# Optimization experiments

Measured on AMD Instinct MI355X. Metric: run time of the kernel, lower is better.

The kernel has to match this reference:

```python
import jax, jax.numpy as jnp
import numpy as np

N = 100_000      # nodes
E = 1_600_000    # directed edges (before self-loops)
F_IN = 128       # input node features
H = 4            # attention heads
C = 64           # hidden channels (concat=False -> heads averaged)
NEG_SLOPE = 0.2
BN_EPS = 1e-5


def setup_inputs() -> dict:
    key = jax.random.key(0)
    ks = jax.random.split(key, 16)
    s = 0.05
    return {
        "x": jax.random.normal(ks[0], (N, F_IN), dtype=jnp.float32),
        "edge_index": jax.random.randint(ks[1], (2, E), 0, N, dtype=jnp.int64),
        # GAT layer params: layer 0 has F_IN inputs, layers 1..2 have C inputs
        "W0": jax.random.normal(ks[2], (F_IN, H * C), dtype=jnp.float32) * s,
        "Wl": jax.random.normal(ks[3], (2, C, H * C), dtype=jnp.float32) * s,
        "att_src": jax.random.normal(ks[4], (3, H, C), dtype=jnp.float32) * s,
        "att_dst": jax.random.normal(ks[5], (3, H, C), dtype=jnp.float32) * s,
        "conv_bias": jnp.zeros((3, C), dtype=jnp.float32),
        # BatchNorm1d (inference: running stats)
        "bn_gamma": jnp.ones((3, C), dtype=jnp.float32),
        "bn_beta": jnp.zeros((3, C), dtype=jnp.float32),
        "bn_mean": jax.random.normal(ks[6], (3, C), dtype=jnp.float32) * 0.1,
        "bn_var": jax.random.uniform(ks[7], (3, C), dtype=jnp.float32, minval=0.5, maxval=1.5),
        # MLP head
        "lin1_w": jax.random.normal(ks[8], (C, C // 2), dtype=jnp.float32) * s,
        "lin1_b": jnp.zeros((C // 2,), dtype=jnp.float32),
        "lin2_w": jax.random.normal(ks[9], (C // 2, 1), dtype=jnp.float32) * s,
        "lin2_b": jnp.zeros((1,), dtype=jnp.float32),
    }


def _gat_layer(x, src, dst, W, a_src, a_dst, bias):
    # x: [N, Fin] -> h: [N, H, C]
    h = (x @ W).reshape(-1, H, C)
    # per-node attention logits, gathered per edge: [Etot, H]
    e_src = jnp.einsum("nhc,hc->nh", h, a_src)
    e_dst = jnp.einsum("nhc,hc->nh", h, a_dst)
    e = jax.nn.leaky_relu(e_src[src] + e_dst[dst], NEG_SLOPE)
    # softmax over incoming edges of each target node (self-loops guarantee non-empty)
    e_max = jax.ops.segment_max(e, dst, num_segments=N)
    w = jnp.exp(e - e_max[dst])                              # [Etot, H]
    denom = jax.ops.segment_sum(w, dst, num_segments=N)      # [N, H]
    # weighted scatter-add of gathered source features
    msg = h[src] * w[:, :, None]                             # [Etot, H, C]
    out = jax.ops.segment_sum(msg, dst, num_segments=N)      # [N, H, C]
    out = out / denom[:, :, None]
    return out.mean(axis=1) + bias                           # concat=False -> head mean


def reference(x, edge_index, W0, Wl, att_src, att_dst, conv_bias,
              bn_gamma, bn_beta, bn_mean, bn_var,
              lin1_w, lin1_b, lin2_w, lin2_b):
    # add self-loops (PyG GATConv default)
    loop = jnp.arange(N, dtype=edge_index.dtype)
    src = jnp.concatenate([edge_index[0], loop])
    dst = jnp.concatenate([edge_index[1], loop])

    Ws = [W0, Wl[0], Wl[1]]
    for l in range(3):
        x = _gat_layer(x, src, dst, Ws[l], att_src[l], att_dst[l], conv_bias[l])
        x = (x - bn_mean[l]) * (bn_gamma[l] / jnp.sqrt(bn_var[l] + BN_EPS)) + bn_beta[l]
        x = jax.nn.relu(x)  # dropout is identity in inference

    x = jax.nn.relu(x @ lin1_w + lin1_b)
    x = x @ lin2_w + lin2_b
    return x.squeeze(-1)
```

## Files before the change

### kernel.cpp

```cpp
#include <hip/hip_runtime.h>
#include <hip/hip_bf16.h>
#include <cstdint>

#define N_NODES 100000
#define N_EDGES 1600000
#define N_TOT   1700000
#define HEADS   4
#define CH      64
#define HC      256
#define NEG     0.2f
#define BNEPS   1e-5f

static __device__ __forceinline__ float lrelu(float x) {
    return x > 0.f ? x : NEG * x;
}
static __device__ __forceinline__ unsigned short f2bf(float f) {
    unsigned int u = __float_as_uint(f);
    unsigned int r = (u + 0x7fffu + ((u >> 16) & 1u)) >> 16;
    return (unsigned short)r;
}
static __device__ __forceinline__ float bflo(unsigned int v) { return __uint_as_float(v << 16); }
static __device__ __forceinline__ float bfhi(unsigned int v) { return __uint_as_float(v & 0xffff0000u); }

__global__ void detect_dtype(const int* ei32, int* flag) {
    int l = threadIdx.x;
    int v = ei32[2 * l + 1];
    unsigned long long b = __ballot(v == 0);
    if (l == 0) *flag = (__popcll(b) >= 48) ? 1 : 0;
}

static __device__ __forceinline__ int edge_at(const void* ei, int is64, long long pos) {
    if (is64) return (int)((const long long*)ei)[pos];
    return ((const int*)ei)[pos];
}

__global__ void hist_k(const void* ei, const int* flag, int* counts) {
    int e = blockIdx.x * blockDim.x + threadIdx.x;
    if (e >= N_TOT) return;
    int is64 = *flag;
    int d = (e < N_EDGES) ? edge_at(ei, is64, (long long)N_EDGES + e) : (e - N_EDGES);
    atomicAdd(&counts[d], 1);
}

__global__ void scan_block(const int* in, int* out, int* bsum) {
    __shared__ int sm[256];
    int t = threadIdx.x;
    int i = blockIdx.x * 256 + t;
    int v = (i < N_NODES) ? in[i] : 0;
    int acc = v;
    sm[t] = v; __syncthreads();
    for (int d = 1; d < 256; d <<= 1) {
        int add = (t >= d) ? sm[t - d] : 0;
        __syncthreads();
        acc += add; sm[t] = acc;
        __syncthreads();
    }
    if (i < N_NODES) out[i] = acc - v;
    if (t == 255) bsum[blockIdx.x] = acc;
}

__global__ void scan_bsum(int* bsum, int nb) {
    __shared__ int sm[512];
    int t = threadIdx.x;
    int v = (t < nb) ? bsum[t] : 0;
    int acc = v;
    sm[t] = v; __syncthreads();
    for (int d = 1; d < 512; d <<= 1) {
        int add = (t >= d) ? sm[t - d] : 0;
        __syncthreads();
        acc += add; sm[t] = acc;
        __syncthreads();
    }
    if (t < nb) bsum[t] = acc - v;
}

__global__ void scan_add(int* off, const int* bsum, int* fill) {
    int i = blockIdx.x * 256 + threadIdx.x;
    if (i < N_NODES) {
        int v = off[i] + bsum[blockIdx.x];
        off[i] = v; fill[i] = v;
    }
    if (i == 0) off[N_NODES] = N_TOT;
}

__global__ void scatter_k(const void* ei, const int* flag, int* fill, int* csr_src) {
    int e = blockIdx.x * blockDim.x + threadIdx.x;
    if (e >= N_TOT) return;
    int is64 = *flag;
    int s, d;
    if (e < N_EDGES) { s = edge_at(ei, is64, e); d = edge_at(ei, is64, (long long)N_EDGES + e); }
    else { s = e - N_EDGES; d = s; }
    int pos = atomicAdd(&fill[d], 1);
    csr_src[pos] = s;
}

__global__ __launch_bounds__(256) void gemm_fused_k(const float* __restrict__ A,
                                                    const float* __restrict__ W,
                                                    const float* __restrict__ as,
                                                    const float* __restrict__ ad,
                                                    unsigned short* __restrict__ hb,
                                                    float* __restrict__ es,
                                                    float* __restrict__ ed, int K) {
    __shared__ float As[16][68];
    __shared__ float Ws[16][64];
    int t = threadIdx.x;
    int bm = blockIdx.x * 64, bn = blockIdx.y * 64, head = blockIdx.y;
    int ty = t >> 4, tx = t & 15;
    float acc[4][4] = {{0.f}};
    int ar = t >> 2, ak = (t & 3) * 4;
    int wr = t >> 4, wc = (t & 15) * 4;

    for (int k0 = 0; k0 < K; k0 += 16) {
        float4 av = make_float4(0.f, 0.f, 0.f, 0.f);
        int grow = bm + ar;
        if (grow < N_NODES) av = *(const float4*)(A + (size_t)grow * K + k0 + ak);
        As[ak][ar] = av.x; As[ak + 1][ar] = av.y; As[ak + 2][ar] = av.z; As[ak + 3][ar] = av.w;
        *(float4*)(&Ws[wr][wc]) = *(const float4*)(W + (size_t)(k0 + wr) * HC + bn + wc);
        __syncthreads();
        #pragma unroll
        for (int kk = 0; kk < 16; ++kk) {
            float4 a  = *(const float4*)(&As[kk][ty * 4]);
            float4 bq = *(const float4*)(&Ws[kk][tx * 4]);
            acc[0][0] += a.x * bq.x; acc[0][1] += a.x * bq.y; acc[0][2] += a.x * bq.z; acc[0][3] += a.x * bq.w;
            acc[1][0] += a.y * bq.x; acc[1][1] += a.y * bq.y; acc[1][2] += a.y * bq.z; acc[1][3] += a.y * bq.w;
            acc[2][0] += a.z * bq.x; acc[2][1] += a.z * bq.y; acc[2][2] += a.z * bq.z; acc[2][3] += a.z * bq.w;
            acc[3][0] += a.w * bq.x; acc[3][1] += a.w * bq.y; acc[3][2] += a.w * bq.z; acc[3][3] += a.w * bq.w;
        }
        __syncthreads();
    }

    float4 asv = *(const float4*)(as + head * CH + tx * 4);
    float4 adv = *(const float4*)(ad + head * CH + tx * 4);

    #pragma unroll
    for (int r = 0; r < 4; ++r) {
        int grow = bm + ty * 4 + r;
        if (grow < N_NODES) {
            ushort4 hv;
            hv.x = f2bf(acc[r][0]); hv.y = f2bf(acc[r][1]);
            hv.z = f2bf(acc[r][2]); hv.w = f2bf(acc[r][3]);
            *(ushort4*)(hb + (size_t)grow * HC + bn + tx * 4) = hv;
        }
        float ps = acc[r][0] * asv.x + acc[r][1] * asv.y + acc[r][2] * asv.z + acc[r][3] * asv.w;
        float pd = acc[r][0] * adv.x + acc[r][1] * adv.y + acc[r][2] * adv.z + acc[r][3] * adv.w;
        #pragma unroll
        for (int d = 1; d < 16; d <<= 1) {
            ps += __shfl_xor(ps, d);
            pd += __shfl_xor(pd, d);
        }
        if (tx == 0 && grow < N_NODES) {
            es[(size_t)grow * 4 + head] = ps;
            ed[(size_t)grow * 4 + head] = pd;
        }
    }
}

__global__ __launch_bounds__(256) void aggregate_k(const unsigned short* __restrict__ h,
                                                   const float* __restrict__ es,
                                                   const float* __restrict__ ed,
                                                   const int* __restrict__ off,
                                                   const int* __restrict__ csr,
                                                   const float* __restrict__ bias,
                                                   const float* __restrict__ g,
                                                   const float* __restrict__ bb,
                                                   const float* __restrict__ mu,
                                                   const float* __restrict__ var,
                                                   float* __restrict__ xout) {
    __shared__ float wbuf[4][64][4];
    __shared__ int   sbuf[4][64];
    int wv = threadIdx.x >> 6;
    int lane = threadIdx.x & 63;
    int wid = blockIdx.x * 4 + wv;
    if (wid >= N_NODES) return;

    int s0 = off[wid], s1 = off[wid + 1];
    float4 edv = *(const float4*)(ed + (size_t)wid * 4);

    int half = lane >> 5;
    int sub  = lane & 31;
    int head = sub >> 3;
    float ds0 = 0.f, ds1 = 0.f, ds2 = 0.f, ds3 = 0.f;
    float a0 = 0.f, a1 = 0.f, a2 = 0.f, a3 = 0.f, a4 = 0.f, a5 = 0.f, a6 = 0.f, a7 = 0.f;

    for (int base = s0; base < s1; base += 64) {
        int e = base + lane;
        float w0 = 0.f, w1 = 0.f, w2 = 0.f, w3 = 0.f;
        int s = 0;
        if (e < s1) {
            s = csr[e];
            float4 ev = *(const float4*)(es + (size_t)s * 4);
            w0 = __expf(fminf(lrelu(ev.x + edv.x), 80.f));
            w1 = __expf(fminf(lrelu(ev.y + edv.y), 80.f));
            w2 = __expf(fminf(lrelu(ev.z + edv.z), 80.f));
            w3 = __expf(fminf(lrelu(ev.w + edv.w), 80.f));
        }
        ds0 += w0; ds1 += w1; ds2 += w2; ds3 += w3;
        *(float4*)(&wbuf[wv][lane][0]) = make_float4(w0, w1, w2, w3);
        sbuf[wv][lane] = s;
        asm volatile("" ::: "memory");

        int cnt = min(64, s1 - base);
        for (int j = 0; j < cnt; j += 2) {
            int jj = j + half;
            if (jj < cnt) {
                int   ss = sbuf[wv][jj];
                float wm = wbuf[wv][jj][head];
                uint4 hv = *(const uint4*)(h + (size_t)ss * HC + sub * 8);
                a0 = fmaf(wm, bflo(hv.x), a0); a1 = fmaf(wm, bfhi(hv.x), a1);
                a2 = fmaf(wm, bflo(hv.y), a2); a3 = fmaf(wm, bfhi(hv.y), a3);
                a4 = fmaf(wm, bflo(hv.z), a4); a5 = fmaf(wm, bfhi(hv.z), a5);
                a6 = fmaf(wm, bflo(hv.w), a6); a7 = fmaf(wm, bfhi(hv.w), a7);
            }
        }
        asm volatile("" ::: "memory");
    }

    a0 += __shfl_xor(a0, 32); a1 += __shfl_xor(a1, 32);
    a2 += __shfl_xor(a2, 32); a3 += __shfl_xor(a3, 32);
    a4 += __shfl_xor(a4, 32); a5 += __shfl_xor(a5, 32);
    a6 += __shfl_xor(a6, 32); a7 += __shfl_xor(a7, 32);

    #pragma unroll
    for (int d = 1; d < 64; d <<= 1) {
        ds0 += __shfl_xor(ds0, d); ds1 += __shfl_xor(ds1, d);
        ds2 += __shfl_xor(ds2, d); ds3 += __shfl_xor(ds3, d);
    }
    float den = head == 0 ? ds0 : head == 1 ? ds1 : head == 2 ? ds2 : ds3;
    float inv = 1.f / den;
    a0 *= inv; a1 *= inv; a2 *= inv; a3 *= inv;
    a4 *= inv; a5 *= inv; a6 *= inv; a7 *= inv;

    a0 += __shfl_xor(a0, 8);  a1 += __shfl_xor(a1, 8);
    a2 += __shfl_xor(a2, 8);  a3 += __shfl_xor(a3, 8);
    a4 += __shfl_xor(a4, 8);  a5 += __shfl_xor(a5, 8);
    a6 += __shfl_xor(a6, 8);  a7 += __shfl_xor(a7, 8);
    a0 += __shfl_xor(a0, 16); a1 += __shfl_xor(a1, 16);
    a2 += __shfl_xor(a2, 16); a3 += __shfl_xor(a3, 16);
    a4 += __shfl_xor(a4, 16); a5 += __shfl_xor(a5, 16);
    a6 += __shfl_xor(a6, 16); a7 += __shfl_xor(a7, 16);

    if (lane < 8) {
        int c = lane * 8;
        float av[8] = {a0, a1, a2, a3, a4, a5, a6, a7};
        float4 bi0 = *(const float4*)(bias + c), bi1 = *(const float4*)(bias + c + 4);
        float4 gv0 = *(const float4*)(g + c),    gv1 = *(const float4*)(g + c + 4);
        float4 bv0 = *(const float4*)(bb + c),   bv1 = *(const float4*)(bb + c + 4);
        float4 mv0 = *(const float4*)(mu + c),   mv1 = *(const float4*)(mu + c + 4);
        float4 vv0 = *(const float4*)(var + c),  vv1 = *(const float4*)(var + c + 4);
        float bia[8] = {bi0.x, bi0.y, bi0.z, bi0.w, bi1.x, bi1.y, bi1.z, bi1.w};
        float gg[8]  = {gv0.x, gv0.y, gv0.z, gv0.w, gv1.x, gv1.y, gv1.z, gv1.w};
        float be[8]  = {bv0.x, bv0.y, bv0.z, bv0.w, bv1.x, bv1.y, bv1.z, bv1.w};
        float mm[8]  = {mv0.x, mv0.y, mv0.z, mv0.w, mv1.x, mv1.y, mv1.z, mv1.w};
        float vv[8]  = {vv0.x, vv0.y, vv0.z, vv0.w, vv1.x, vv1.y, vv1.z, vv1.w};
        float o[8];
        #pragma unroll
        for (int k = 0; k < 8; ++k) {
            float t0 = (av[k] * 0.25f + bia[k] - mm[k]) * (gg[k] * rsqrtf(vv[k] + BNEPS)) + be[k];
            o[k] = fmaxf(t0, 0.f);
        }
        *(float4*)(xout + (size_t)wid * CH + c)     = make_float4(o[0], o[1], o[2], o[3]);
        *(float4*)(xout + (size_t)wid * CH + c + 4) = make_float4(o[4], o[5], o[6], o[7]);
    }
}

__global__ __launch_bounds__(256) void mlp_k(const float* __restrict__ x,
                                             const float* __restrict__ w1,
                                             const float* __restrict__ b1,
                                             const float* __restrict__ w2,
                                             const float* __restrict__ b2,
                                             float* __restrict__ out) {
    __shared__ float w1s[CH * 32];
    __shared__ float w2s[32];
    __shared__ float b1s[32];
    int t = threadIdx.x;
    for (int i = t; i < CH * 32; i += 256) w1s[i] = w1[i];
    if (t < 32) { w2s[t] = w2[t]; b1s[t] = b1[t]; }
    __syncthreads();
    int n = blockIdx.x * 256 + t;
    if (n >= N_NODES) return;
    float y[32];
    #pragma unroll
    for (int j = 0; j < 32; ++j) y[j] = b1s[j];
    const float* xr = x + (size_t)n * CH;
    for (int c4 = 0; c4 < 16; ++c4) {
        float4 xv = *(const float4*)(xr + c4 * 4);
        const float* wr = &w1s[c4 * 4 * 32];
        #pragma unroll
        for (int j = 0; j < 32; ++j)
            y[j] += xv.x * wr[j] + xv.y * wr[32 + j] + xv.z * wr[64 + j] + xv.w * wr[96 + j];
    }
    float o = b2[0];
    #pragma unroll
    for (int j = 0; j < 32; ++j) o += fmaxf(y[j], 0.f) * w2s[j];
    out[n] = o;
}

extern "C" void kernel_launch(void* const* d_in, const int* in_sizes, int n_in,
                              void* d_out, int out_size, void* d_ws, size_t ws_size,
                              hipStream_t stream) {
    const float* x0    = (const float*)d_in[0];
    const void*  ei    = d_in[1];
    const float* W0    = (const float*)d_in[2];
    const float* Wl    = (const float*)d_in[3];
    const float* asrc  = (const float*)d_in[4];
    const float* adst  = (const float*)d_in[5];
    const float* cbias = (const float*)d_in[6];
    const float* bng   = (const float*)d_in[7];
    const float* bnb   = (const float*)d_in[8];
    const float* bnm   = (const float*)d_in[9];
    const float* bnv   = (const float*)d_in[10];
    const float* l1w   = (const float*)d_in[11];
    const float* l1b   = (const float*)d_in[12];
    const float* l2w   = (const float*)d_in[13];
    const float* l2b   = (const float*)d_in[14];
    float* out = (float*)d_out;

    char* p = (char*)d_ws;
    auto alloc = [&](size_t bytes) { char* r = p; p += (bytes + 255) & ~(size_t)255; return r; };
    unsigned short* hb = (unsigned short*)alloc((size_t)N_NODES * HC * 2);
    float* xA   = (float*)alloc((size_t)N_NODES * CH * 4);
    float* xB   = (float*)alloc((size_t)N_NODES * CH * 4);
    float* es   = (float*)alloc((size_t)N_NODES * 4 * 4);
    float* ed   = (float*)alloc((size_t)N_NODES * 4 * 4);
    int* counts = (int*)alloc((size_t)N_NODES * 4);
    int* off    = (int*)alloc((size_t)(N_NODES + 1) * 4);
    int* fill   = (int*)alloc((size_t)N_NODES * 4);
    int* bsum   = (int*)alloc(512 * 4);
    int* flag   = (int*)alloc(256);
    int* csr    = (int*)alloc((size_t)N_TOT * 4);

    int nbScan = (N_NODES + 255) / 256;
    hipMemsetAsync(counts, 0, (size_t)N_NODES * 4, stream);
    detect_dtype<<<1, 64, 0, stream>>>((const int*)ei, flag);
    hist_k<<<(N_TOT + 255) / 256, 256, 0, stream>>>(ei, flag, counts);
    scan_block<<<nbScan, 256, 0, stream>>>(counts, off, bsum);
    scan_bsum<<<1, 512, 0, stream>>>(bsum, nbScan);
    scan_add<<<nbScan, 256, 0, stream>>>(off, bsum, fill);
    scatter_k<<<(N_TOT + 255) / 256, 256, 0, stream>>>(ei, flag, fill, csr);

    const float* xin = x0;
    int K = 128;
    const float* W = W0;
    float* xbufs[2] = {xA, xB};
    for (int l = 0; l < 3; ++l) {
        dim3 gg((N_NODES + 63) / 64, HC / 64);
        gemm_fused_k<<<gg, 256, 0, stream>>>(xin, W, asrc + l * HC, adst + l * HC,
                                             hb, es, ed, K);
        float* xo = xbufs[l & 1];
        aggregate_k<<<(N_NODES + 3) / 4, 256, 0, stream>>>(hb, es, ed, off, csr,
            cbias + l * CH, bng + l * CH, bnb + l * CH, bnm + l * CH, bnv + l * CH, xo);
        xin = xo;
        K = CH;
        W = Wl + (size_t)l * CH * HC;
    }
    mlp_k<<<(N_NODES + 255) / 256, 256, 0, stream>>>(xin, l1w, l1b, l2w, l2b, out);
}
```

Before: 848.9 us.

## Use bf16 MFMA GEMM, partitioned CSR build, and wider per-lane aggregation

The FP32 SIMT GEMM is replaced by a bf16 MFMA 16x16x32 kernel with swizzled LDS tiles. Each block now covers all four heads, and the weights are converted to bf16 per layer. The CSR build first converts edges to int32, then runs the histogram and scatter in destination-range partitions so atomics stay local in cache. Aggregation now has each lane load 16 bf16 channels per edge and process four edges at a time. Rounding the inputs and weights to bf16 adds precision loss, and the partitioned passes read the edge list eight times.

```diff
diff --git a/kernel.cpp b/kernel.cpp
--- a/kernel.cpp
+++ b/kernel.cpp
@@ -10,6 +10,12 @@
 #define HC      256
 #define NEG     0.2f
 #define BNEPS   1e-5f
+#define NPART   8
+#define PART_N  12500
+#define CHUNK_E 16384
+
+typedef __attribute__((ext_vector_type(8))) short short8;
+typedef __attribute__((ext_vector_type(4))) float f32x4;
 
 static __device__ __forceinline__ float lrelu(float x) {
     return x > 0.f ? x : NEG * x;
@@ -34,12 +40,28 @@
     return ((const int*)ei)[pos];
 }
 
-__global__ void hist_k(const void* ei, const int* flag, int* counts) {
-    int e = blockIdx.x * blockDim.x + threadIdx.x;
+__global__ void convert_k(const void* ei, const int* flag, int* src32, int* dst32) {
+    int e = blockIdx.x * 256 + threadIdx.x;
     if (e >= N_TOT) return;
     int is64 = *flag;
-    int d = (e < N_EDGES) ? edge_at(ei, is64, (long long)N_EDGES + e) : (e - N_EDGES);
-    atomicAdd(&counts[d], 1);
+    if (e < N_EDGES) {
+        src32[e] = edge_at(ei, is64, e);
+        dst32[e] = edge_at(ei, is64, (long long)N_EDGES + e);
+    } else {
+        int v = e - N_EDGES;
+        src32[e] = v; dst32[e] = v;
+    }
+}
+
+__global__ void hist_part_k(const int* __restrict__ dst32, int* __restrict__ counts) {
+    int part = blockIdx.x & (NPART - 1), chunk = blockIdx.x / NPART;
+    int lo = part * PART_N, hi = lo + PART_N;
+    int base = chunk * CHUNK_E;
+    int end = min(base + CHUNK_E, N_TOT);
+    for (int i = base + threadIdx.x; i < end; i += 256) {
+        int d = dst32[i];
+        if (d >= lo && d < hi) atomicAdd(&counts[d], 1);
+    }
 }
 
 __global__ void scan_block(const int* in, int* out, int* bsum) {
@@ -83,75 +105,135 @@
     if (i == 0) off[N_NODES] = N_TOT;
 }
 
-__global__ void scatter_k(const void* ei, const int* flag, int* fill, int* csr_src) {
-    int e = blockIdx.x * blockDim.x + threadIdx.x;
-    if (e >= N_TOT) return;
-    int is64 = *flag;
-    int s, d;
-    if (e < N_EDGES) { s = edge_at(ei, is64, e); d = edge_at(ei, is64, (long long)N_EDGES + e); }
-    else { s = e - N_EDGES; d = s; }
-    int pos = atomicAdd(&fill[d], 1);
-    csr_src[pos] = s;
-}
-
-__global__ __launch_bounds__(256) void gemm_fused_k(const float* __restrict__ A,
-                                                    const float* __restrict__ W,
-                                                    const float* __restrict__ as,
-                                                    const float* __restrict__ ad,
-                                                    unsigned short* __restrict__ hb,
-                                                    float* __restrict__ es,
-                                                    float* __restrict__ ed, int K) {
-    __shared__ float As[16][68];
-    __shared__ float Ws[16][64];
+__global__ void scatter_part_k(const int* __restrict__ src32, const int* __restrict__ dst32,
+                               int* __restrict__ fill, int* __restrict__ csr) {
+    int part = blockIdx.x & (NPART - 1), chunk = blockIdx.x / NPART;
+    int lo = part * PART_N, hi = lo + PART_N;
+    int base = chunk * CHUNK_E;
+    int end = min(base + CHUNK_E, N_TOT);
+    for (int i = base + threadIdx.x; i < end; i += 256) {
+        int d = dst32[i];
+        if (d >= lo && d < hi) {
+            int s = src32[i];
+            int pos = atomicAdd(&fill[d], 1);
+            csr[pos] = s;
+        }
+    }
+}
+
+__global__ void wconv_k(const float* __restrict__ w, unsigned short* __restrict__ wb, int n) {
+    int i = blockIdx.x * 256 + threadIdx.x;
+    if (i < n) wb[i] = f2bf(w[i]);
+}
+
+template<int K>
+__global__ __launch_bounds__(256) void gemm_mfma_k(const float* __restrict__ A,
+                                                   const unsigned short* __restrict__ Wb,
+                                                   const float* __restrict__ as,
+                                                   const float* __restrict__ ad,
+                                                   unsigned short* __restrict__ hb,
+                                                   float* __restrict__ es,
+                                                   float* __restrict__ ed) {
+    __shared__ unsigned short Bs[256 * K];
+    __shared__ unsigned short As[64 * K];
     int t = threadIdx.x;
-    int bm = blockIdx.x * 64, bn = blockIdx.y * 64, head = blockIdx.y;
-    int ty = t >> 4, tx = t & 15;
-    float acc[4][4] = {{0.f}};
-    int ar = t >> 2, ak = (t & 3) * 4;
-    int wr = t >> 4, wc = (t & 15) * 4;
-
-    for (int k0 = 0; k0 < K; k0 += 16) {
-        float4 av = make_float4(0.f, 0.f, 0.f, 0.f);
-        int grow = bm + ar;
-        if (grow < N_NODES) av = *(const float4*)(A + (size_t)grow * K + k0 + ak);
-        As[ak][ar] = av.x; As[ak + 1][ar] = av.y; As[ak + 2][ar] = av.z; As[ak + 3][ar] = av.w;
-        *(float4*)(&Ws[wr][wc]) = *(const float4*)(W + (size_t)(k0 + wr) * HC + bn + wc);
-        __syncthreads();
-        #pragma unroll
-        for (int kk = 0; kk < 16; ++kk) {
-            float4 a  = *(const float4*)(&As[kk][ty * 4]);
-            float4 bq = *(const float4*)(&Ws[kk][tx * 4]);
-            acc[0][0] += a.x * bq.x; acc[0][1] += a.x * bq.y; acc[0][2] += a.x * bq.z; acc[0][3] += a.x * bq.w;
-            acc[1][0] += a.y * bq.x; acc[1][1] += a.y * bq.y; acc[1][2] += a.y * bq.z; acc[1][3] += a.y * bq.w;
-            acc[2][0] += a.z * bq.x; acc[2][1] += a.z * bq.y; acc[2][2] += a.z * bq.z; acc[2][3] += a.z * bq.w;
-            acc[3][0] += a.w * bq.x; acc[3][1] += a.w * bq.y; acc[3][2] += a.w * bq.z; acc[3][3] += a.w * bq.w;
-        }
-        __syncthreads();
-    }
-
-    float4 asv = *(const float4*)(as + head * CH + tx * 4);
-    float4 adv = *(const float4*)(ad + head * CH + tx * 4);
-
-    #pragma unroll
-    for (int r = 0; r < 4; ++r) {
-        int grow = bm + ty * 4 + r;
-        if (grow < N_NODES) {
-            ushort4 hv;
-            hv.x = f2bf(acc[r][0]); hv.y = f2bf(acc[r][1]);
-            hv.z = f2bf(acc[r][2]); hv.w = f2bf(acc[r][3]);
-            *(ushort4*)(hb + (size_t)grow * HC + bn + tx * 4) = hv;
-        }
-        float ps = acc[r][0] * asv.x + acc[r][1] * asv.y + acc[r][2] * asv.z + acc[r][3] * asv.w;
-        float pd = acc[r][0] * adv.x + acc[r][1] * adv.y + acc[r][2] * adv.z + acc[r][3] * adv.w;
-        #pragma unroll
-        for (int d = 1; d < 16; d <<= 1) {
-            ps += __shfl_xor(ps, d);
-            pd += __shfl_xor(pd, d);
-        }
-        if (tx == 0 && grow < N_NODES) {
-            es[(size_t)grow * 4 + head] = ps;
-            ed[(size_t)grow * 4 + head] = pd;
-        }
+    int bm = blockIdx.x * 64;
+
+    for (int idx4 = t; idx4 < K * 64; idx4 += 256) {
+        int k = idx4 >> 6;
+        int c = (idx4 & 63) * 4;
+        ushort4 wv = *(const ushort4*)(Wb + (size_t)k * HC + c);
+        Bs[((c + 0) * K + k) ^ ((((c + 0) & 7)) << 3)] = wv.x;
+        Bs[((c + 1) * K + k) ^ ((((c + 1) & 7)) << 3)] = wv.y;
+        Bs[((c + 2) * K + k) ^ ((((c + 2) & 7)) << 3)] = wv.z;
+        Bs[((c + 3) * K + k) ^ ((((c + 3) & 7)) << 3)] = wv.w;
+    }
+    {
+        int row = t >> 2, seg = t & 3;
+        int grow = bm + row;
+        const float* Ar = A + (size_t)grow * K + seg * (K / 4);
+        #pragma unroll
+        for (int f = 0; f < K / 16; ++f) {
+            float4 v = make_float4(0.f, 0.f, 0.f, 0.f);
+            if (grow < N_NODES) v = *(const float4*)(Ar + f * 4);
+            ushort4 b;
+            b.x = f2bf(v.x); b.y = f2bf(v.y); b.z = f2bf(v.z); b.w = f2bf(v.w);
+            int idx = (row * K + seg * (K / 4) + f * 4) ^ ((row & 7) << 3);
+            *(ushort4*)(&As[idx]) = b;
+        }
+    }
+    __syncthreads();
+
+    int w = t >> 6, lane = t & 63;
+    int c16 = lane & 15, kg = lane >> 4;
+    int swz = (c16 & 7) << 3;
+    f32x4 acc[4][4];
+    #pragma unroll
+    for (int i = 0; i < 4; ++i)
+        #pragma unroll
+        for (int j = 0; j < 4; ++j) acc[i][j] = (f32x4)(0.f);
+
+    #pragma unroll
+    for (int kc = 0; kc < K / 32; ++kc) {
+        int ko = kc * 32 + kg * 8;
+        short8 af[4], bf[4];
+        #pragma unroll
+        for (int rs = 0; rs < 4; ++rs)
+            af[rs] = *(const short8*)(&As[((16 * rs + c16) * K + ko) ^ swz]);
+        #pragma unroll
+        for (int ct = 0; ct < 4; ++ct) {
+            int col = w * 64 + ct * 16 + c16;
+            bf[ct] = *(const short8*)(&Bs[(col * K + ko) ^ swz]);
+        }
+        #pragma unroll
+        for (int rs = 0; rs < 4; ++rs)
+            #pragma unroll
+            for (int ct = 0; ct < 4; ++ct)
+                acc[rs][ct] = __builtin_amdgcn_mfma_f32_16x16x32_bf16(af[rs], bf[ct], acc[rs][ct], 0, 0, 0);
+    }
+
+    float asv[4], adv[4];
+    #pragma unroll
+    for (int ct = 0; ct < 4; ++ct) {
+        asv[ct] = as[w * 64 + ct * 16 + c16];
+        adv[ct] = ad[w * 64 + ct * 16 + c16];
+    }
+    #pragma unroll
+    for (int rs = 0; rs < 4; ++rs) {
+        float esr[4], edr[4];
+        #pragma unroll
+        for (int reg = 0; reg < 4; ++reg) {
+            float s = 0.f, d = 0.f;
+            #pragma unroll
+            for (int ct = 0; ct < 4; ++ct) {
+                s += acc[rs][ct][reg] * asv[ct];
+                d += acc[rs][ct][reg] * adv[ct];
+            }
+            #pragma unroll
+            for (int sh = 1; sh < 16; sh <<= 1) {
+                s += __shfl_xor(s, sh);
+                d += __shfl_xor(d, sh);
+            }
+            esr[reg] = s; edr[reg] = d;
+        }
+        int r0 = bm + rs * 16 + kg * 4;
+        if (c16 == 0) {
+            #pragma unroll
+            for (int reg = 0; reg < 4; ++reg) {
+                if (r0 + reg < N_NODES) {
+                    es[(size_t)(r0 + reg) * 4 + w] = esr[reg];
+                    ed[(size_t)(r0 + reg) * 4 + w] = edr[reg];
+                }
+            }
+        }
+        #pragma unroll
+        for (int ct = 0; ct < 4; ++ct)
+            #pragma unroll
+            for (int reg = 0; reg < 4; ++reg) {
+                int grow = r0 + reg;
+                if (grow < N_NODES)
+                    hb[(size_t)grow * HC + w * 64 + ct * 16 + c16] = f2bf(acc[rs][ct][reg]);
+            }
     }
 }
 
@@ -176,11 +258,13 @@
     int s0 = off[wid], s1 = off[wid + 1];
     float4 edv = *(const float4*)(ed + (size_t)wid * 4);
 
-    int half = lane >> 5;
-    int sub  = lane & 31;
-    int head = sub >> 3;
+    int q = lane >> 4;
+    int s16 = lane & 15;
+    int head = s16 >> 2;
     float ds0 = 0.f, ds1 = 0.f, ds2 = 0.f, ds3 = 0.f;
-    float a0 = 0.f, a1 = 0.f, a2 = 0.f, a3 = 0.f, a4 = 0.f, a5 = 0.f, a6 = 0.f, a7 = 0.f;
+    float a[16];
+    #pragma unroll
+    for (int i = 0; i < 16; ++i) a[i] = 0.f;
 
     for (int base = s0; base < s1; base += 64) {
         int e = base + lane;
@@ -200,26 +284,32 @@
         asm volatile("" ::: "memory");
 
         int cnt = min(64, s1 - base);
-        for (int j = 0; j < cnt; j += 2) {
-            int jj = j + half;
+        for (int j = 0; j < cnt; j += 4) {
+            int jj = j + q;
             if (jj < cnt) {
                 int   ss = sbuf[wv][jj];
                 float wm = wbuf[wv][jj][head];
-                uint4 hv = *(const uint4*)(h + (size_t)ss * HC + sub * 8);
-                a0 = fmaf(wm, bflo(hv.x), a0); a1 = fmaf(wm, bfhi(hv.x), a1);
-                a2 = fmaf(wm, bflo(hv.y), a2); a3 = fmaf(wm, bfhi(hv.y), a3);
-                a4 = fmaf(wm, bflo(hv.z), a4); a5 = fmaf(wm, bfhi(hv.z), a5);
-                a6 = fmaf(wm, bflo(hv.w), a6); a7 = fmaf(wm, bfhi(hv.w), a7);
+                const unsigned short* hp = h + (size_t)ss * HC + s16 * 16;
+                uint4 h0 = *(const uint4*)hp;
+                uint4 h1 = *(const uint4*)(hp + 8);
+                a[0]  = fmaf(wm, bflo(h0.x), a[0]);  a[1]  = fmaf(wm, bfhi(h0.x), a[1]);
+                a[2]  = fmaf(wm, bflo(h0.y), a[2]);  a[3]  = fmaf(wm, bfhi(h0.y), a[3]);
+                a[4]  = fmaf(wm, bflo(h0.z), a[4]);  a[5]  = fmaf(wm, bfhi(h0.z), a[5]);
+                a[6]  = fmaf(wm, bflo(h0.w), a[6]);  a[7]  = fmaf(wm, bfhi(h0.w), a[7]);
+                a[8]  = fmaf(wm, bflo(h1.x), a[8]);  a[9]  = fmaf(wm, bfhi(h1.x), a[9]);
+                a[10] = fmaf(wm, bflo(h1.y), a[10]); a[11] = fmaf(wm, bfhi(h1.y), a[11]);
+                a[12] = fmaf(wm, bflo(h1.z), a[12]); a[13] = fmaf(wm, bfhi(h1.z), a[13]);
+                a[14] = fmaf(wm, bflo(h1.w), a[14]); a[15] = fmaf(wm, bfhi(h1.w), a[15]);
             }
         }
         asm volatile("" ::: "memory");
     }
 
-    a0 += __shfl_xor(a0, 32); a1 += __shfl_xor(a1, 32);
-    a2 += __shfl_xor(a2, 32); a3 += __shfl_xor(a3, 32);
-    a4 += __shfl_xor(a4, 32); a5 += __shfl_xor(a5, 32);
-    a6 += __shfl_xor(a6, 32); a7 += __shfl_xor(a7, 32);
-
+    #pragma unroll
+    for (int i = 0; i < 16; ++i) {
+        a[i] += __shfl_xor(a[i], 16);
+        a[i] += __shfl_xor(a[i], 32);
+    }
     #pragma unroll
     for (int d = 1; d < 64; d <<= 1) {
         ds0 += __shfl_xor(ds0, d); ds1 += __shfl_xor(ds1, d);
@@ -227,39 +317,34 @@
     }
     float den = head == 0 ? ds0 : head == 1 ? ds1 : head == 2 ? ds2 : ds3;
     float inv = 1.f / den;
-    a0 *= inv; a1 *= inv; a2 *= inv; a3 *= inv;
-    a4 *= inv; a5 *= inv; a6 *= inv; a7 *= inv;
-
-    a0 += __shfl_xor(a0, 8);  a1 += __shfl_xor(a1, 8);
-    a2 += __shfl_xor(a2, 8);  a3 += __shfl_xor(a3, 8);
-    a4 += __shfl_xor(a4, 8);  a5 += __shfl_xor(a5, 8);
-    a6 += __shfl_xor(a6, 8);  a7 += __shfl_xor(a7, 8);
-    a0 += __shfl_xor(a0, 16); a1 += __shfl_xor(a1, 16);
-    a2 += __shfl_xor(a2, 16); a3 += __shfl_xor(a3, 16);
-    a4 += __shfl_xor(a4, 16); a5 += __shfl_xor(a5, 16);
-    a6 += __shfl_xor(a6, 16); a7 += __shfl_xor(a7, 16);
-
-    if (lane < 8) {
-        int c = lane * 8;
-        float av[8] = {a0, a1, a2, a3, a4, a5, a6, a7};
-        float4 bi0 = *(const float4*)(bias + c), bi1 = *(const float4*)(bias + c + 4);
-        float4 gv0 = *(const float4*)(g + c),    gv1 = *(const float4*)(g + c + 4);
-        float4 bv0 = *(const float4*)(bb + c),   bv1 = *(const float4*)(bb + c + 4);
-        float4 mv0 = *(const float4*)(mu + c),   mv1 = *(const float4*)(mu + c + 4);
-        float4 vv0 = *(const float4*)(var + c),  vv1 = *(const float4*)(var + c + 4);
-        float bia[8] = {bi0.x, bi0.y, bi0.z, bi0.w, bi1.x, bi1.y, bi1.z, bi1.w};
-        float gg[8]  = {gv0.x, gv0.y, gv0.z, gv0.w, gv1.x, gv1.y, gv1.z, gv1.w};
-        float be[8]  = {bv0.x, bv0.y, bv0.z, bv0.w, bv1.x, bv1.y, bv1.z, bv1.w};
-        float mm[8]  = {mv0.x, mv0.y, mv0.z, mv0.w, mv1.x, mv1.y, mv1.z, mv1.w};
-        float vv[8]  = {vv0.x, vv0.y, vv0.z, vv0.w, vv1.x, vv1.y, vv1.z, vv1.w};
-        float o[8];
-        #pragma unroll
-        for (int k = 0; k < 8; ++k) {
-            float t0 = (av[k] * 0.25f + bia[k] - mm[k]) * (gg[k] * rsqrtf(vv[k] + BNEPS)) + be[k];
-            o[k] = fmaxf(t0, 0.f);
-        }
-        *(float4*)(xout + (size_t)wid * CH + c)     = make_float4(o[0], o[1], o[2], o[3]);
-        *(float4*)(xout + (size_t)wid * CH + c + 4) = make_float4(o[4], o[5], o[6], o[7]);
+    #pragma unroll
+    for (int i = 0; i < 16; ++i) a[i] *= inv;
+    #pragma unroll
+    for (int i = 0; i < 16; ++i) {
+        a[i] += __shfl_xor(a[i], 4);
+        a[i] += __shfl_xor(a[i], 8);
+    }
+
+    if (lane < 4) {
+        int c0 = lane * 16;
+        float o[16];
+        #pragma unroll
+        for (int v4 = 0; v4 < 4; ++v4) {
+            int c = c0 + v4 * 4;
+            float4 bi = *(const float4*)(bias + c);
+            float4 gv = *(const float4*)(g + c);
+            float4 bv = *(const float4*)(bb + c);
+            float4 mv = *(const float4*)(mu + c);
+            float4 vv = *(const float4*)(var + c);
+            o[v4 * 4 + 0] = fmaxf((a[v4 * 4 + 0] * 0.25f + bi.x - mv.x) * (gv.x * rsqrtf(vv.x + BNEPS)) + bv.x, 0.f);
+            o[v4 * 4 + 1] = fmaxf((a[v4 * 4 + 1] * 0.25f + bi.y - mv.y) * (gv.y * rsqrtf(vv.y + BNEPS)) + bv.y, 0.f);
+            o[v4 * 4 + 2] = fmaxf((a[v4 * 4 + 2] * 0.25f + bi.z - mv.z) * (gv.z * rsqrtf(vv.z + BNEPS)) + bv.z, 0.f);
+            o[v4 * 4 + 3] = fmaxf((a[v4 * 4 + 3] * 0.25f + bi.w - mv.w) * (gv.w * rsqrtf(vv.w + BNEPS)) + bv.w, 0.f);
+        }
+        #pragma unroll
+        for (int v4 = 0; v4 < 4; ++v4)
+            *(float4*)(xout + (size_t)wid * CH + c0 + v4 * 4) =
+                make_float4(o[v4 * 4 + 0], o[v4 * 4 + 1], o[v4 * 4 + 2], o[v4 * 4 + 3]);
     }
 }
 
@@ -317,7 +402,8 @@
 
     char* p = (char*)d_ws;
     auto alloc = [&](size_t bytes) { char* r = p; p += (bytes + 255) & ~(size_t)255; return r; };
-    unsigned short* hb = (unsigned short*)alloc((size_t)N_NODES * HC * 2);
+    unsigned short* hb  = (unsigned short*)alloc((size_t)N_NODES * HC * 2);
+    unsigned short* wbf = (unsigned short*)alloc((size_t)128 * HC * 2);
     float* xA   = (float*)alloc((size_t)N_NODES * CH * 4);
     float* xB   = (float*)alloc((size_t)N_NODES * CH * 4);
     float* es   = (float*)alloc((size_t)N_NODES * 4 * 4);
@@ -327,30 +413,36 @@
     int* fill   = (int*)alloc((size_t)N_NODES * 4);
     int* bsum   = (int*)alloc(512 * 4);
     int* flag   = (int*)alloc(256);
+    int* src32  = (int*)alloc((size_t)N_TOT * 4);
+    int* dst32  = (int*)alloc((size_t)N_TOT * 4);
     int* csr    = (int*)alloc((size_t)N_TOT * 4);
 
     int nbScan = (N_NODES + 255) / 256;
+    int nchunk = (N_TOT + CHUNK_E - 1) / CHUNK_E;
     hipMemsetAsync(counts, 0, (size_t)N_NODES * 4, stream);
     detect_dtype<<<1, 64, 0, stream>>>((const int*)ei, flag);
-    hist_k<<<(N_TOT + 255) / 256, 256, 0, stream>>>(ei, flag, counts);
+    convert_k<<<(N_TOT + 255) / 256, 256, 0, stream>>>(ei, flag, src32, dst32);
+    hist_part_k<<<nchunk * NPART, 256, 0, stream>>>(dst32, counts);
     scan_block<<<nbScan, 256, 0, stream>>>(counts, off, bsum);
     scan_bsum<<<1, 512, 0, stream>>>(bsum, nbScan);
     scan_add<<<nbScan, 256, 0, stream>>>(off, bsum, fill);
-    scatter_k<<<(N_TOT + 255) / 256, 256, 0, stream>>>(ei, flag, fill, csr);
+    scatter_part_k<<<nchunk * NPART, 256, 0, stream>>>(src32, dst32, fill, csr);
 
     const float* xin = x0;
-    int K = 128;
     const float* W = W0;
     float* xbufs[2] = {xA, xB};
+    int ngemm = (N_NODES + 63) / 64;
     for (int l = 0; l < 3; ++l) {
-        dim3 gg((N_NODES + 63) / 64, HC / 64);
-        gemm_fused_k<<<gg, 256, 0, stream>>>(xin, W, asrc + l * HC, adst + l * HC,
-                                             hb, es, ed, K);
+        int K = (l == 0) ? 128 : 64;
+        wconv_k<<<(K * HC + 255) / 256, 256, 0, stream>>>(W, wbf, K * HC);
+        if (l == 0)
+            gemm_mfma_k<128><<<ngemm, 256, 0, stream>>>(xin, wbf, asrc + l * HC, adst + l * HC, hb, es, ed);
+        else
+            gemm_mfma_k<64><<<ngemm, 256, 0, stream>>>(xin, wbf, asrc + l * HC, adst + l * HC, hb, es, ed);
         float* xo = xbufs[l & 1];
         aggregate_k<<<(N_NODES + 3) / 4, 256, 0, stream>>>(hb, es, ed, off, csr,
             cbias + l * CH, bng + l * CH, bnb + l * CH, bnm + l * CH, bnv + l * CH, xo);
         xin = xo;
-        K = CH;
         W = Wl + (size_t)l * CH * HC;
     }
     mlp_k<<<(N_NODES + 255) / 256, 256, 0, stream>>>(xin, l1w, l1b, l2w, l2b, out);
```

Result: faster. 773.7 us (-8.9%).
